# Kernel optimization log

Hardware: AMD Instinct MI355X
Metric: run time of the kernel (lower is better)

Reference implementation:

```python
import jax, jax.numpy as jnp
import numpy as np

NEG = -1e9  # stand-in for -inf in masked_fill; avoids NaN rows for never-gathered states


def _residual(x, w1, b1, w2, b2):
    # ResidualLayerOld: two relu linears with a residual connection (eval mode, no dropout)
    h = jax.nn.relu(x @ w1.T + b1)
    return x + jax.nn.relu(h @ w2.T + b2)


def setup_inputs() -> dict:
    key = jax.random.key(0)
    B, T, V, C, H, SPW = 16, 256, 32000, 1024, 512, 8
    ks = jax.random.split(key, 32)
    s = 0.05  # keep logits in a sane range
    inp = {
        'start_emb': jax.random.normal(ks[0], (C, H), jnp.float32) * s,
        'start_l1w': jax.random.normal(ks[1], (H, H), jnp.float32) * s,
        'start_l1b': jnp.zeros((H,), jnp.float32),
        'start_l2w': jax.random.normal(ks[2], (H, H), jnp.float32) * s,
        'start_l2b': jnp.zeros((H,), jnp.float32),
        'start_ow': jax.random.normal(ks[3], (1, H), jnp.float32) * s,
        'start_ob': jnp.zeros((1,), jnp.float32),
        'state_emb': jax.random.normal(ks[4], (C, H), jnp.float32) * s,
        'trans_l1w': jax.random.normal(ks[5], (H, H), jnp.float32) * s,
        'trans_l1b': jnp.zeros((H,), jnp.float32),
        'trans_l2w': jax.random.normal(ks[6], (H, H), jnp.float32) * s,
        'trans_l2b': jnp.zeros((H,), jnp.float32),
        'proj_w': jax.random.normal(ks[7], (C, H), jnp.float32) * s,
        'pret_emb': jax.random.normal(ks[8], (C, H), jnp.float32) * s,
        'term_l1w': jax.random.normal(ks[9], (H, H), jnp.float32) * s,
        'term_l1b': jnp.zeros((H,), jnp.float32),
        'term_l2w': jax.random.normal(ks[10], (H, H), jnp.float32) * s,
        'term_l2b': jnp.zeros((H,), jnp.float32),
        'term_ow': jax.random.normal(ks[11], (V, H), jnp.float32) * s,
        'term_ob': jnp.zeros((V,), jnp.float32),
        'text': jax.random.randint(ks[12], (B, T), 0, V, jnp.int32),
        'word2state': jax.random.randint(ks[13], (V, SPW), 0, C, jnp.int32),
    }
    return inp


def reference(start_emb, start_l1w, start_l1b, start_l2w, start_l2b, start_ow, start_ob,
              state_emb, trans_l1w, trans_l1b, trans_l2w, trans_l2b, proj_w,
              pret_emb, term_l1w, term_l1b, term_l2w, term_l2b, term_ow, term_ob,
              text, word2state):
    C, H = start_emb.shape
    V, SPW = word2state.shape

    # start: MLP(C,H)->(C,1) -> log_softmax over C
    start = jax.nn.log_softmax(
        (_residual(start_emb, start_l1w, start_l1b, start_l2w, start_l2b) @ start_ow.T + start_ob).squeeze(-1))

    # transition: [C,C] log_softmax over next state
    trans = jax.nn.log_softmax(
        _residual(state_emb, trans_l1w, trans_l1b, trans_l2w, trans_l2b) @ proj_w.T, axis=-1)

    # emission: [C,V] logits, masked to the sparse word->state assignment, log_softmax over V
    term_logits = _residual(pret_emb, term_l1w, term_l1b, term_l2w, term_l2b) @ term_ow.T + term_ob
    mask = jnp.zeros((C, V), bool).at[word2state.reshape(-1), jnp.repeat(jnp.arange(V), SPW)].set(True)
    emission = jax.nn.log_softmax(jnp.where(mask, term_logits, NEG), axis=-1)

    # clamp: gather per-timestep [SPW,SPW] transition blocks + emissions
    cs = word2state[text]                               # [B,T,SPW]
    pot = trans[cs[:, :-1, :, None], cs[:, 1:, None, :]]  # [B,T-1,SPW,SPW] (prev i, next j)
    init = start[cs[:, 0]]                              # [B,SPW]
    obs = emission[cs, text[:, :, None]]                # [B,T,SPW]
    pot = pot.at[:, 0].add((init + obs[:, 0])[:, :, None])
    pot = pot + obs[:, 1:][:, :, None, :]               # add obs_{t+1} along next-state j
    pot = jnp.swapaxes(pot, -1, -2)                     # [B,T-1,next,prev], as in clamp()

    # forward algorithm (fb kernel's alpha pass): alpha_{t+1}[n] = LSE_p pot[t,n,p] + alpha_t[p]
    def step(alpha, p):
        a = jax.nn.logsumexp(p + alpha[:, None, :], axis=-1)
        return a, None

    B = text.shape[0]
    alpha0 = jnp.zeros((B, SPW), pot.dtype)
    alphaT, _ = jax.lax.scan(step, alpha0, jnp.swapaxes(pot, 0, 1))
    evidence = jax.nn.logsumexp(alphaT, axis=-1).sum()  # full-length sequences
    return evidence
```

## Files before the change

### kernel.cpp

```cpp
#include <hip/hip_runtime.h>
#include <hip/hip_bf16.h>

#define C_DIM 1024
#define H_DIM 512
#define V_DIM 32000
#define B_DIM 16
#define T_DIM 256
#define SPW   8
#define NSLOT 32

typedef unsigned short u16;
typedef unsigned int   u32;
typedef __attribute__((ext_vector_type(8))) short bf16x8;
typedef __attribute__((ext_vector_type(4))) float f32x4;

__device__ __forceinline__ u16 f2b(float f) {
    union { float f; u32 i; } x; x.f = f;
    u32 i = x.i;
    i += 0x7fffu + ((i >> 16) & 1u);
    return (u16)(i >> 16);
}
__device__ __forceinline__ float b2f(u16 u) {
    union { u32 i; float f; } x; x.i = ((u32)u) << 16; return x.f;
}
__device__ __forceinline__ float dot8_bf16(uint4 u, const float4 tw0, const float4 tw1) {
    return tw0.x * b2f((u16)(u.x & 0xffff)) + tw0.y * b2f((u16)(u.x >> 16))
         + tw0.z * b2f((u16)(u.y & 0xffff)) + tw0.w * b2f((u16)(u.y >> 16))
         + tw1.x * b2f((u16)(u.z & 0xffff)) + tw1.y * b2f((u16)(u.z >> 16))
         + tw1.z * b2f((u16)(u.w & 0xffff)) + tw1.w * b2f((u16)(u.w >> 16));
}

struct CvtArgs {
    const float* src[10];
    u16*         dst[10];
    int          n[10];
    float*       zero;
    int          zn;
};

__global__ __launch_bounds__(256) void cvt_kern(CvtArgs a)
{
    int seg = blockIdx.y;
    if (seg == 10) {
        for (int i = blockIdx.x * 256 + threadIdx.x; i < a.zn; i += gridDim.x * 256)
            a.zero[i] = 0.0f;
        return;
    }
    const float4* s = (const float4*)a.src[seg];
    ushort4* d = (ushort4*)a.dst[seg];
    int n4 = a.n[seg] >> 2;
    for (int i = blockIdx.x * 256 + threadIdx.x; i < n4; i += gridDim.x * 256) {
        float4 v = s[i];
        ushort4 o;
        o.x = f2b(v.x); o.y = f2b(v.y); o.z = f2b(v.z); o.w = f2b(v.w);
        d[i] = o;
    }
}

struct MlpArgs {
    const u16*   A[3];
    const u16*   W[3];
    const float* bias[3];
    const float* resid[3];
    u16*         out[3];
};

__global__ __launch_bounds__(256) void mlp16_kern(MlpArgs args)
{
    const int N = H_DIM, K = H_DIM;
    int z = blockIdx.z;
    const u16* A = args.A[z];
    const u16* B = args.W[z];
    const float* bias = args.bias[z];
    const float* resid = args.resid[z];
    u16* out = args.out[z];

    __shared__ __align__(16) u16 As[2][64][40];
    __shared__ __align__(16) u16 Bs[2][64][40];
    int tid  = threadIdx.x;
    int m0 = blockIdx.x * 64, n0 = blockIdx.y * 64;
    int wave = tid >> 6, lane = tid & 63;
    int wr = wave >> 1, wc = wave & 1;
    int srow = tid >> 2, scol = (tid & 3) << 3;
    int quad = lane >> 4, l16 = lane & 15;
    f32x4 acc[2][2] = {};

    const u16* ap = A + (size_t)(m0 + srow) * K + scol;
    const u16* bp = B + (size_t)(n0 + srow) * K + scol;

    *(uint4*)&As[0][srow][scol] = *(const uint4*)ap;
    *(uint4*)&Bs[0][srow][scol] = *(const uint4*)bp;
    __syncthreads();
    int cur = 0;
#pragma unroll 1
    for (int k0 = 0; k0 + 32 < K; k0 += 32) {
        uint4 an = *(const uint4*)(ap + k0 + 32);
        uint4 bn = *(const uint4*)(bp + k0 + 32);
        bf16x8 af0 = *(const bf16x8*)&As[cur][wr * 32 + l16][quad * 8];
        bf16x8 af1 = *(const bf16x8*)&As[cur][wr * 32 + 16 + l16][quad * 8];
        bf16x8 bf0 = *(const bf16x8*)&Bs[cur][wc * 32 + l16][quad * 8];
        bf16x8 bf1 = *(const bf16x8*)&Bs[cur][wc * 32 + 16 + l16][quad * 8];
        acc[0][0] = __builtin_amdgcn_mfma_f32_16x16x32_bf16(af0, bf0, acc[0][0], 0, 0, 0);
        acc[0][1] = __builtin_amdgcn_mfma_f32_16x16x32_bf16(af0, bf1, acc[0][1], 0, 0, 0);
        acc[1][0] = __builtin_amdgcn_mfma_f32_16x16x32_bf16(af1, bf0, acc[1][0], 0, 0, 0);
        acc[1][1] = __builtin_amdgcn_mfma_f32_16x16x32_bf16(af1, bf1, acc[1][1], 0, 0, 0);
        *(uint4*)&As[cur ^ 1][srow][scol] = an;
        *(uint4*)&Bs[cur ^ 1][srow][scol] = bn;
        __syncthreads();
        cur ^= 1;
    }
    {
        bf16x8 af0 = *(const bf16x8*)&As[cur][wr * 32 + l16][quad * 8];
        bf16x8 af1 = *(const bf16x8*)&As[cur][wr * 32 + 16 + l16][quad * 8];
        bf16x8 bf0 = *(const bf16x8*)&Bs[cur][wc * 32 + l16][quad * 8];
        bf16x8 bf1 = *(const bf16x8*)&Bs[cur][wc * 32 + 16 + l16][quad * 8];
        acc[0][0] = __builtin_amdgcn_mfma_f32_16x16x32_bf16(af0, bf0, acc[0][0], 0, 0, 0);
        acc[0][1] = __builtin_amdgcn_mfma_f32_16x16x32_bf16(af0, bf1, acc[0][1], 0, 0, 0);
        acc[1][0] = __builtin_amdgcn_mfma_f32_16x16x32_bf16(af1, bf0, acc[1][0], 0, 0, 0);
        acc[1][1] = __builtin_amdgcn_mfma_f32_16x16x32_bf16(af1, bf1, acc[1][1], 0, 0, 0);
    }
#pragma unroll
    for (int sm = 0; sm < 2; sm++)
#pragma unroll
        for (int sn = 0; sn < 2; sn++) {
            int n = n0 + wc * 32 + sn * 16 + l16;
            float bv = bias[n];
#pragma unroll
            for (int reg = 0; reg < 4; reg++) {
                int m = m0 + wr * 32 + sm * 16 + quad * 4 + reg;
                float v = fmaxf(acc[sm][sn][reg] + bv, 0.0f);
                if (resid) v += resid[(size_t)m * N + n];
                out[(size_t)m * N + n] = f2b(v);
            }
        }
}

__global__ __launch_bounds__(256) void fused_mid_kern(
    const u16* __restrict__ Rtrans16, const u16* __restrict__ proj16,
    float* __restrict__ TL, float* __restrict__ rowsum,
    const u16* __restrict__ Rterm16, const float* __restrict__ tow,
    const float* __restrict__ tob, const int* __restrict__ w2s,
    float* __restrict__ Zpart, float* __restrict__ Lmat,
    const u16* __restrict__ Rstart16, const float* __restrict__ sow,
    const float* __restrict__ sob, float* __restrict__ startv,
    float* __restrict__ Ssum)
{
    __shared__ __align__(16) u16 As[2][64][40];
    __shared__ __align__(16) u16 Bs[2][64][40];
    int bx = blockIdx.x;
    int tid = threadIdx.x;
    int wid = tid >> 6, lane = tid & 63;

    if (bx < 256) {
        const int K = H_DIM;
        int m0 = (bx & 15) * 64, n0 = (bx >> 4) * 64;
        int wave = wid;
        int wr = wave >> 1, wc = wave & 1;
        int srow = tid >> 2, scol = (tid & 3) << 3;
        int quad = lane >> 4, l16 = lane & 15;
        f32x4 acc[2][2] = {};

        const u16* ap = Rtrans16 + (size_t)(m0 + srow) * K + scol;
        const u16* bp = proj16 + (size_t)(n0 + srow) * K + scol;

        *(uint4*)&As[0][srow][scol] = *(const uint4*)ap;
        *(uint4*)&Bs[0][srow][scol] = *(const uint4*)bp;
        __syncthreads();
        int cur = 0;
#pragma unroll 1
        for (int k0 = 0; k0 + 32 < K; k0 += 32) {
            uint4 an = *(const uint4*)(ap + k0 + 32);
            uint4 bn = *(const uint4*)(bp + k0 + 32);
            bf16x8 af0 = *(const bf16x8*)&As[cur][wr * 32 + l16][quad * 8];
            bf16x8 af1 = *(const bf16x8*)&As[cur][wr * 32 + 16 + l16][quad * 8];
            bf16x8 bf0 = *(const bf16x8*)&Bs[cur][wc * 32 + l16][quad * 8];
            bf16x8 bf1 = *(const bf16x8*)&Bs[cur][wc * 32 + 16 + l16][quad * 8];
            acc[0][0] = __builtin_amdgcn_mfma_f32_16x16x32_bf16(af0, bf0, acc[0][0], 0, 0, 0);
            acc[0][1] = __builtin_amdgcn_mfma_f32_16x16x32_bf16(af0, bf1, acc[0][1], 0, 0, 0);
            acc[1][0] = __builtin_amdgcn_mfma_f32_16x16x32_bf16(af1, bf0, acc[1][0], 0, 0, 0);
            acc[1][1] = __builtin_amdgcn_mfma_f32_16x16x32_bf16(af1, bf1, acc[1][1], 0, 0, 0);
            *(uint4*)&As[cur ^ 1][srow][scol] = an;
            *(uint4*)&Bs[cur ^ 1][srow][scol] = bn;
            __syncthreads();
            cur ^= 1;
        }
        {
            bf16x8 af0 = *(const bf16x8*)&As[cur][wr * 32 + l16][quad * 8];
            bf16x8 af1 = *(const bf16x8*)&As[cur][wr * 32 + 16 + l16][quad * 8];
            bf16x8 bf0 = *(const bf16x8*)&Bs[cur][wc * 32 + l16][quad * 8];
            bf16x8 bf1 = *(const bf16x8*)&Bs[cur][wc * 32 + 16 + l16][quad * 8];
            acc[0][0] = __builtin_amdgcn_mfma_f32_16x16x32_bf16(af0, bf0, acc[0][0], 0, 0, 0);
            acc[0][1] = __builtin_amdgcn_mfma_f32_16x16x32_bf16(af0, bf1, acc[0][1], 0, 0, 0);
            acc[1][0] = __builtin_amdgcn_mfma_f32_16x16x32_bf16(af1, bf0, acc[1][0], 0, 0, 0);
            acc[1][1] = __builtin_amdgcn_mfma_f32_16x16x32_bf16(af1, bf1, acc[1][1], 0, 0, 0);
        }
#pragma unroll
        for (int sm = 0; sm < 2; sm++)
#pragma unroll
            for (int reg = 0; reg < 4; reg++) {
                int m = m0 + wr * 32 + sm * 16 + quad * 4 + reg;
                float e = 0.0f;
#pragma unroll
                for (int sn = 0; sn < 2; sn++) {
                    int n = n0 + wc * 32 + sn * 16 + l16;
                    float v = acc[sm][sn][reg];
                    TL[(size_t)m * C_DIM + n] = v;
                    e += expf(v);
                }
                e += __shfl_xor(e, 1, 64);
                e += __shfl_xor(e, 2, 64);
                e += __shfl_xor(e, 4, 64);
                e += __shfl_xor(e, 8, 64);
                if (l16 == 0) atomicAdd(rowsum + m, e);
            }
        return;
    }

    if (bx < 256 + V_DIM / 4) {
        int vbid = bx - 256;
        int v = vbid * 4 + wid;
        float* slot = Zpart + (vbid & (NSLOT - 1)) * C_DIM;
        const float4* twp = (const float4*)(tow + (size_t)v * H_DIM);
        float4 tw0 = twp[lane * 2], tw1 = twp[lane * 2 + 1];
        float ob = tob[v];
        int cs[SPW];
#pragma unroll
        for (int s = 0; s < SPW; s++) cs[s] = w2s[v * SPW + s];
        uint4 rv[SPW];
#pragma unroll
        for (int s = 0; s < SPW; s++)
            rv[s] = ((const uint4*)(Rterm16 + (size_t)cs[s] * H_DIM))[lane];
        float d[SPW];
#pragma unroll
        for (int s = 0; s < SPW; s++) {
            d[s] = dot8_bf16(rv[s], tw0, tw1);
            d[s] += __shfl_xor(d[s], 1, 64);
            d[s] += __shfl_xor(d[s], 2, 64);
            d[s] += __shfl_xor(d[s], 4, 64);
        }
        float x = d[0];
        int myc = cs[0];
#pragma unroll
        for (int s = 1; s < SPW; s++) {
            if ((lane & 7) == s) { x = d[s]; myc = cs[s]; }
        }
        x += __shfl_xor(x, 8, 64);
        x += __shfl_xor(x, 16, 64);
        x += __shfl_xor(x, 32, 64);
        u32 dupmask = 0;
#pragma unroll
        for (int s = 1; s < SPW; s++) {
            bool dp = false;
#pragma unroll
            for (int s2 = 0; s2 < s; s2++) dp = dp || (cs[s2] == cs[s]);
            if (dp) dupmask |= (1u << s);
        }
        if (lane < 8) {
            Lmat[(size_t)v * SPW + lane] = x + ob;
            if (!((dupmask >> lane) & 1u))
                atomicAdd(slot + myc, expf(x + ob));
        }
        return;
    }

    int sbid = bx - (256 + V_DIM / 4);
    int c = sbid * 4 + wid;
    uint4 rv = ((const uint4*)(Rstart16 + (size_t)c * H_DIM))[lane];
    const float4* wp = (const float4*)(sow);
    float4 w0 = wp[lane * 2], w1 = wp[lane * 2 + 1];
    float d = dot8_bf16(rv, w0, w1);
    for (int off = 1; off < 64; off <<= 1) d += __shfl_xor(d, off, 64);
    if (lane == 0) {
        d += sob[0];
        startv[c] = d;
        atomicAdd(Ssum + (sbid & (NSLOT - 1)), expf(d));
    }
}

__global__ __launch_bounds__(256) void zred_kern(
    const float* __restrict__ Zpart, const float* __restrict__ rowsum,
    float* __restrict__ logZ, float* __restrict__ logrow)
{
    int c = blockIdx.x * 256 + threadIdx.x;
    float z = 0.0f;
#pragma unroll
    for (int k = 0; k < NSLOT; k++) z += Zpart[(size_t)k * C_DIM + c];
    logZ[c] = logf(z);
    logrow[c] = logf(rowsum[c]);
}

__device__ __forceinline__ float lsm_combine(float accv, float mv, int i, int j)
{
    float x[8];
#pragma unroll
    for (int k = 0; k < 8; k++) {
        float a = __shfl(accv, k * 8 + i, 64);
        float b = __shfl(mv,  j * 8 + k, 64);
        x[k] = a + b;
    }
    float mx = fmaxf(fmaxf(fmaxf(x[0], x[1]), fmaxf(x[2], x[3])),
                     fmaxf(fmaxf(x[4], x[5]), fmaxf(x[6], x[7])));
    float s = 0.0f;
#pragma unroll
    for (int k = 0; k < 8; k++) s += expf(x[k] - mx);
    return mx + logf(s);
}

__global__ __launch_bounds__(64) void scanA_kern(
    const float* __restrict__ TL, const float* __restrict__ logrow,
    const float* __restrict__ Lmat, const float* __restrict__ logZ,
    const float* __restrict__ startv, const float* __restrict__ Ssum,
    const int* __restrict__ text, const int* __restrict__ w2s,
    float* __restrict__ Mc)
{
    int lane = threadIdx.x;
    int g = blockIdx.x;
    int b = g >> 4, c = g & 15;
    int t0 = c * 16;
    int cnt = min(16, (T_DIM - 1) - t0);
    int i = lane & 7, j = lane >> 3;

    const int* txt = text + b * T_DIM;

    float logS = 0.0f;
    if (t0 == 0) {
        float ss = 0.0f;
#pragma unroll
        for (int k = 0; k < NSLOT; k++) ss += Ssum[k];
        logS = logf(ss);
    }

    auto potval = [&](int t) -> float {
        int vt  = txt[t];
        int vt1 = txt[t + 1];
        int ci = w2s[vt * SPW + i];
        int cj = w2s[vt1 * SPW + j];
        float p = TL[(size_t)ci * C_DIM + cj] - logrow[ci]
                + Lmat[(size_t)vt1 * SPW + j] - logZ[cj];
        if (t == 0)
            p += startv[ci] - logS + Lmat[(size_t)vt * SPW + i] - logZ[ci];
        return p;
    };

    float acc = potval(t0);
    if (cnt > 1) {
        float nv = potval(t0 + 1);
        for (int t = t0 + 1; t < t0 + cnt; t++) {
            float nv2 = (t + 1 < t0 + cnt) ? potval(t + 1) : 0.0f;
            acc = lsm_combine(acc, nv, i, j);
            nv = nv2;
        }
    }
    Mc[(size_t)g * 64 + lane] = acc;
}

__global__ __launch_bounds__(1024) void scanB_kern(const float* __restrict__ Mc,
                                                   float* __restrict__ out)
{
    int wave = threadIdx.x >> 6, lane = threadIdx.x & 63;
    int i = lane & 7, j = lane >> 3;
    const float* base = Mc + (size_t)wave * 16 * 64;
    float acc = base[lane];
    for (int c = 1; c < 16; c++)
        acc = lsm_combine(acc, base[(size_t)c * 64 + lane], i, j);
    float mx = acc;
    for (int o = 1; o < 64; o <<= 1) mx = fmaxf(mx, __shfl_xor(mx, o, 64));
    float e = expf(acc - mx);
    for (int o = 1; o < 64; o <<= 1) e += __shfl_xor(e, o, 64);
    __shared__ float part[16];
    if (lane == 0) part[wave] = mx + logf(e);
    __syncthreads();
    if (threadIdx.x == 0) {
        float s = 0.0f;
#pragma unroll
        for (int k = 0; k < 16; k++) s += part[k];
        out[0] = s;
    }
}

extern "C" void kernel_launch(void* const* d_in, const int* in_sizes, int n_in,
                              void* d_out, int out_size, void* d_ws, size_t ws_size,
                              hipStream_t stream)
{
    const float* start_emb = (const float*)d_in[0];
    const float* start_l1w = (const float*)d_in[1];
    const float* start_l1b = (const float*)d_in[2];
    const float* start_l2w = (const float*)d_in[3];
    const float* start_l2b = (const float*)d_in[4];
    const float* start_ow  = (const float*)d_in[5];
    const float* start_ob  = (const float*)d_in[6];
    const float* state_emb = (const float*)d_in[7];
    const float* trans_l1w = (const float*)d_in[8];
    const float* trans_l1b = (const float*)d_in[9];
    const float* trans_l2w = (const float*)d_in[10];
    const float* trans_l2b = (const float*)d_in[11];
    const float* proj_w    = (const float*)d_in[12];
    const float* pret_emb  = (const float*)d_in[13];
    const float* term_l1w  = (const float*)d_in[14];
    const float* term_l1b  = (const float*)d_in[15];
    const float* term_l2w  = (const float*)d_in[16];
    const float* term_l2b  = (const float*)d_in[17];
    const float* term_ow   = (const float*)d_in[18];
    const float* term_ob   = (const float*)d_in[19];
    const int*   text      = (const int*)d_in[20];
    const int*   w2s       = (const int*)d_in[21];

    char* w = (char*)d_ws;
    const u32 MB = 1u << 20;
    const size_t CH = (size_t)C_DIM * H_DIM;
    const size_t HH = (size_t)H_DIM * H_DIM;

    u16*   emb16  = (u16*)(w);
    u16*   w16    = (u16*)(w + 3u * MB);
    u16*   proj16 = (u16*)(w + 6u * MB);
    u16*   H16    = (u16*)(w + 7u * MB);
    u16*   R16    = (u16*)(w + 10u * MB);
    float* TL     = (float*)(w + 13u * MB);
    float* startv = (float*)(w + 17u * MB);
    float* logZ   = (float*)(w + 17u * MB + 4096);
    float* logrow = (float*)(w + 17u * MB + 8192);
    float* Mc     = (float*)(w + 17u * MB + 12288);
    float* Zpart  = (float*)(w + 18u * MB);
    float* Ssum   = Zpart + (size_t)NSLOT * C_DIM;
    float* rowsum = Ssum + NSLOT;
    float* Lmat   = (float*)(w + 19u * MB);

    u16* semb16 = emb16;
    u16* temb16 = emb16 + CH;
    u16* pemb16 = emb16 + 2 * CH;
    u16* sl1w16 = w16;
    u16* sl2w16 = w16 + HH;
    u16* tl1w16 = w16 + 2 * HH;
    u16* tl2w16 = w16 + 3 * HH;
    u16* ml1w16 = w16 + 4 * HH;
    u16* ml2w16 = w16 + 5 * HH;
    u16* Hs = H16, *Ht = H16 + CH, *Hp = H16 + 2 * CH;
    u16* Rstart16 = R16;
    u16* Rtrans16 = R16 + CH;
    u16* Rterm16  = R16 + 2 * CH;

    dim3 blk256(256);

    CvtArgs cv;
    cv.src[0] = start_emb; cv.dst[0] = semb16; cv.n[0] = (int)CH;
    cv.src[1] = state_emb; cv.dst[1] = temb16; cv.n[1] = (int)CH;
    cv.src[2] = pret_emb;  cv.dst[2] = pemb16; cv.n[2] = (int)CH;
    cv.src[3] = start_l1w; cv.dst[3] = sl1w16; cv.n[3] = (int)HH;
    cv.src[4] = start_l2w; cv.dst[4] = sl2w16; cv.n[4] = (int)HH;
    cv.src[5] = trans_l1w; cv.dst[5] = tl1w16; cv.n[5] = (int)HH;
    cv.src[6] = trans_l2w; cv.dst[6] = tl2w16; cv.n[6] = (int)HH;
    cv.src[7] = term_l1w;  cv.dst[7] = ml1w16; cv.n[7] = (int)HH;
    cv.src[8] = term_l2w;  cv.dst[8] = ml2w16; cv.n[8] = (int)HH;
    cv.src[9] = proj_w;    cv.dst[9] = proj16; cv.n[9] = (int)CH;
    cv.zero = Zpart; cv.zn = NSLOT * C_DIM + NSLOT + C_DIM;
    cvt_kern<<<dim3(128, 11), blk256, 0, stream>>>(cv);

    MlpArgs l1;
    l1.A[0] = semb16; l1.A[1] = temb16; l1.A[2] = pemb16;
    l1.W[0] = sl1w16; l1.W[1] = tl1w16; l1.W[2] = ml1w16;
    l1.bias[0] = start_l1b; l1.bias[1] = trans_l1b; l1.bias[2] = term_l1b;
    l1.resid[0] = nullptr; l1.resid[1] = nullptr; l1.resid[2] = nullptr;
    l1.out[0] = Hs; l1.out[1] = Ht; l1.out[2] = Hp;

    MlpArgs l2;
    l2.A[0] = Hs; l2.A[1] = Ht; l2.A[2] = Hp;
    l2.W[0] = sl2w16; l2.W[1] = tl2w16; l2.W[2] = ml2w16;
    l2.bias[0] = start_l2b; l2.bias[1] = trans_l2b; l2.bias[2] = term_l2b;
    l2.resid[0] = start_emb; l2.resid[1] = state_emb; l2.resid[2] = pret_emb;
    l2.out[0] = Rstart16; l2.out[1] = Rtrans16; l2.out[2] = Rterm16;

    mlp16_kern<<<dim3(16, 8, 3), blk256, 0, stream>>>(l1);
    mlp16_kern<<<dim3(16, 8, 3), blk256, 0, stream>>>(l2);

    fused_mid_kern<<<256 + V_DIM / 4 + C_DIM / 4, blk256, 0, stream>>>(
        Rtrans16, proj16, TL, rowsum,
        Rterm16, term_ow, term_ob, w2s, Zpart, Lmat,
        Rstart16, start_ow, start_ob, startv, Ssum);

    zred_kern<<<C_DIM / 256, blk256, 0, stream>>>(Zpart, rowsum, logZ, logrow);

    scanA_kern<<<B_DIM * 16, dim3(64), 0, stream>>>(TL, logrow, Lmat, logZ,
                                                    startv, Ssum, text, w2s, Mc);
    scanB_kern<<<1, 1024, 0, stream>>>(Mc, (float*)d_out);
}
```

Baseline: 226.0 us.

## Restructure pipeline: fold conversions into MLP, drop zred, finer scan segments

Moves the layer-2 weight and proj bf16 conversion into an extra z-slice of the first MLP launch, so it runs alongside the GEMM. The zred kernel is removed: scanA blocks each rebuild the log-normalisers in shared memory from a transposed Zpart layout. The vocabulary pass now handles two words per wave, and the fast __expf/__logf intrinsics replace expf/logf. Scan parallelism doubles to 32 segments per sequence with a per-batch tree reduction and an atomic add to the output. This trades redundant per-block normaliser work and lower-precision math for fewer launches and more parallelism.

```diff
diff --git a/kernel.cpp b/kernel.cpp
--- a/kernel.cpp
+++ b/kernel.cpp
@@ -8,6 +8,7 @@
 #define T_DIM 256
 #define SPW   8
 #define NSLOT 32
+#define NSEG  32
 
 typedef unsigned short u16;
 typedef unsigned int   u32;
@@ -31,19 +32,21 @@
 }
 
 struct CvtArgs {
-    const float* src[10];
-    u16*         dst[10];
-    int          n[10];
+    const float* src[6];
+    u16*         dst[6];
+    int          n[6];
     float*       zero;
     int          zn;
+    float*       out;
 };
 
 __global__ __launch_bounds__(256) void cvt_kern(CvtArgs a)
 {
     int seg = blockIdx.y;
-    if (seg == 10) {
+    if (seg == 6) {
         for (int i = blockIdx.x * 256 + threadIdx.x; i < a.zn; i += gridDim.x * 256)
             a.zero[i] = 0.0f;
+        if (blockIdx.x == 0 && threadIdx.x == 0) a.out[0] = 0.0f;
         return;
     }
     const float4* s = (const float4*)a.src[seg];
@@ -63,10 +66,30 @@
     const float* bias[3];
     const float* resid[3];
     u16*         out[3];
+    const float* csrc[4];
+    u16*         cdst[4];
+    int          cn[4];
 };
 
 __global__ __launch_bounds__(256) void mlp16_kern(MlpArgs args)
 {
+    if (blockIdx.z == 3) {
+        int idx = (blockIdx.y * gridDim.x + blockIdx.x) * 256 + threadIdx.x;
+        int stride = gridDim.x * gridDim.y * 256;
+#pragma unroll
+        for (int s = 0; s < 4; s++) {
+            const float4* sp = (const float4*)args.csrc[s];
+            ushort4* dp = (ushort4*)args.cdst[s];
+            int n4 = args.cn[s] >> 2;
+            for (int t = idx; t < n4; t += stride) {
+                float4 v = sp[t];
+                ushort4 o;
+                o.x = f2b(v.x); o.y = f2b(v.y); o.z = f2b(v.z); o.w = f2b(v.w);
+                dp[t] = o;
+            }
+        }
+        return;
+    }
     const int N = H_DIM, K = H_DIM;
     int z = blockIdx.z;
     const u16* A = args.A[z];
@@ -154,8 +177,7 @@
     if (bx < 256) {
         const int K = H_DIM;
         int m0 = (bx & 15) * 64, n0 = (bx >> 4) * 64;
-        int wave = wid;
-        int wr = wave >> 1, wc = wave & 1;
+        int wr = wid >> 1, wc = wid & 1;
         int srow = tid >> 2, scol = (tid & 3) << 3;
         int quad = lane >> 4, l16 = lane & 15;
         f32x4 acc[2][2] = {};
@@ -205,7 +227,7 @@
                     int n = n0 + wc * 32 + sn * 16 + l16;
                     float v = acc[sm][sn][reg];
                     TL[(size_t)m * C_DIM + n] = v;
-                    e += expf(v);
+                    e += __expf(v);
                 }
                 e += __shfl_xor(e, 1, 64);
                 e += __shfl_xor(e, 2, 64);
@@ -216,54 +238,57 @@
         return;
     }
 
-    if (bx < 256 + V_DIM / 4) {
-        int vbid = bx - 256;
-        int v = vbid * 4 + wid;
-        float* slot = Zpart + (vbid & (NSLOT - 1)) * C_DIM;
-        const float4* twp = (const float4*)(tow + (size_t)v * H_DIM);
-        float4 tw0 = twp[lane * 2], tw1 = twp[lane * 2 + 1];
-        float ob = tob[v];
-        int cs[SPW];
-#pragma unroll
-        for (int s = 0; s < SPW; s++) cs[s] = w2s[v * SPW + s];
-        uint4 rv[SPW];
-#pragma unroll
-        for (int s = 0; s < SPW; s++)
-            rv[s] = ((const uint4*)(Rterm16 + (size_t)cs[s] * H_DIM))[lane];
-        float d[SPW];
-#pragma unroll
-        for (int s = 0; s < SPW; s++) {
-            d[s] = dot8_bf16(rv[s], tw0, tw1);
-            d[s] += __shfl_xor(d[s], 1, 64);
-            d[s] += __shfl_xor(d[s], 2, 64);
-            d[s] += __shfl_xor(d[s], 4, 64);
-        }
-        float x = d[0];
-        int myc = cs[0];
-#pragma unroll
-        for (int s = 1; s < SPW; s++) {
-            if ((lane & 7) == s) { x = d[s]; myc = cs[s]; }
-        }
-        x += __shfl_xor(x, 8, 64);
-        x += __shfl_xor(x, 16, 64);
-        x += __shfl_xor(x, 32, 64);
-        u32 dupmask = 0;
-#pragma unroll
-        for (int s = 1; s < SPW; s++) {
-            bool dp = false;
-#pragma unroll
-            for (int s2 = 0; s2 < s; s2++) dp = dp || (cs[s2] == cs[s]);
-            if (dp) dupmask |= (1u << s);
-        }
-        if (lane < 8) {
-            Lmat[(size_t)v * SPW + lane] = x + ob;
-            if (!((dupmask >> lane) & 1u))
-                atomicAdd(slot + myc, expf(x + ob));
+    if (bx < 256 + V_DIM / 8) {
+        int qbid = bx - 256;
+        int slotid = qbid & (NSLOT - 1);
+#pragma unroll
+        for (int h = 0; h < 2; h++) {
+            int v = (qbid * 4 + wid) * 2 + h;
+            const float4* twp = (const float4*)(tow + (size_t)v * H_DIM);
+            float4 tw0 = twp[lane * 2], tw1 = twp[lane * 2 + 1];
+            float ob = tob[v];
+            int cs[SPW];
+#pragma unroll
+            for (int s = 0; s < SPW; s++) cs[s] = w2s[v * SPW + s];
+            uint4 rv[SPW];
+#pragma unroll
+            for (int s = 0; s < SPW; s++)
+                rv[s] = ((const uint4*)(Rterm16 + (size_t)cs[s] * H_DIM))[lane];
+            float d[SPW];
+#pragma unroll
+            for (int s = 0; s < SPW; s++) {
+                d[s] = dot8_bf16(rv[s], tw0, tw1);
+                d[s] += __shfl_xor(d[s], 1, 64);
+                d[s] += __shfl_xor(d[s], 2, 64);
+                d[s] += __shfl_xor(d[s], 4, 64);
+            }
+            float x = d[0];
+            int myc = cs[0];
+#pragma unroll
+            for (int s = 1; s < SPW; s++) {
+                if ((lane & 7) == s) { x = d[s]; myc = cs[s]; }
+            }
+            x += __shfl_xor(x, 8, 64);
+            x += __shfl_xor(x, 16, 64);
+            x += __shfl_xor(x, 32, 64);
+            u32 dupmask = 0;
+#pragma unroll
+            for (int s = 1; s < SPW; s++) {
+                bool dp = false;
+#pragma unroll
+                for (int s2 = 0; s2 < s; s2++) dp = dp || (cs[s2] == cs[s]);
+                if (dp) dupmask |= (1u << s);
+            }
+            if (lane < 8) {
+                Lmat[(size_t)v * SPW + lane] = x + ob;
+                if (!((dupmask >> lane) & 1u))
+                    atomicAdd(Zpart + (size_t)myc * NSLOT + slotid, __expf(x + ob));
+            }
         }
         return;
     }
 
-    int sbid = bx - (256 + V_DIM / 4);
+    int sbid = bx - (256 + V_DIM / 8);
     int c = sbid * 4 + wid;
     uint4 rv = ((const uint4*)(Rstart16 + (size_t)c * H_DIM))[lane];
     const float4* wp = (const float4*)(sow);
@@ -273,20 +298,8 @@
     if (lane == 0) {
         d += sob[0];
         startv[c] = d;
-        atomicAdd(Ssum + (sbid & (NSLOT - 1)), expf(d));
-    }
-}
-
-__global__ __launch_bounds__(256) void zred_kern(
-    const float* __restrict__ Zpart, const float* __restrict__ rowsum,
-    float* __restrict__ logZ, float* __restrict__ logrow)
-{
-    int c = blockIdx.x * 256 + threadIdx.x;
-    float z = 0.0f;
-#pragma unroll
-    for (int k = 0; k < NSLOT; k++) z += Zpart[(size_t)k * C_DIM + c];
-    logZ[c] = logf(z);
-    logrow[c] = logf(rowsum[c]);
+        atomicAdd(Ssum + (sbid & (NSLOT - 1)), __expf(d));
+    }
 }
 
 __device__ __forceinline__ float lsm_combine(float accv, float mv, int i, int j)
@@ -302,22 +315,37 @@
                      fmaxf(fmaxf(x[4], x[5]), fmaxf(x[6], x[7])));
     float s = 0.0f;
 #pragma unroll
-    for (int k = 0; k < 8; k++) s += expf(x[k] - mx);
-    return mx + logf(s);
+    for (int k = 0; k < 8; k++) s += __expf(x[k] - mx);
+    return mx + __logf(s);
 }
 
 __global__ __launch_bounds__(64) void scanA_kern(
-    const float* __restrict__ TL, const float* __restrict__ logrow,
-    const float* __restrict__ Lmat, const float* __restrict__ logZ,
+    const float* __restrict__ TL, const float* __restrict__ rowsum,
+    const float* __restrict__ Lmat, const float* __restrict__ Zpart,
     const float* __restrict__ startv, const float* __restrict__ Ssum,
     const int* __restrict__ text, const int* __restrict__ w2s,
     float* __restrict__ Mc)
 {
+    __shared__ float sLZ[C_DIM];
+    __shared__ float sLR[C_DIM];
     int lane = threadIdx.x;
+    for (int c = lane; c < C_DIM; c += 64) {
+        const float4* zp = (const float4*)(Zpart + (size_t)c * NSLOT);
+        float4 z0 = zp[0], z1 = zp[1], z2 = zp[2], z3 = zp[3];
+        float4 z4 = zp[4], z5 = zp[5], z6 = zp[6], z7 = zp[7];
+        float z = ((z0.x + z0.y + z0.z + z0.w) + (z1.x + z1.y + z1.z + z1.w))
+                + ((z2.x + z2.y + z2.z + z2.w) + (z3.x + z3.y + z3.z + z3.w))
+                + ((z4.x + z4.y + z4.z + z4.w) + (z5.x + z5.y + z5.z + z5.w))
+                + ((z6.x + z6.y + z6.z + z6.w) + (z7.x + z7.y + z7.z + z7.w));
+        sLZ[c] = __logf(z);
+        sLR[c] = __logf(rowsum[c]);
+    }
+    __syncthreads();
+
     int g = blockIdx.x;
-    int b = g >> 4, c = g & 15;
-    int t0 = c * 16;
-    int cnt = min(16, (T_DIM - 1) - t0);
+    int b = g >> 5, c = g & (NSEG - 1);
+    int t0 = c * ((T_DIM) / NSEG);
+    int cnt = min(T_DIM / NSEG, (T_DIM - 1) - t0);
     int i = lane & 7, j = lane >> 3;
 
     const int* txt = text + b * T_DIM;
@@ -327,7 +355,7 @@
         float ss = 0.0f;
 #pragma unroll
         for (int k = 0; k < NSLOT; k++) ss += Ssum[k];
-        logS = logf(ss);
+        logS = __logf(ss);
     }
 
     auto potval = [&](int t) -> float {
@@ -335,10 +363,10 @@
         int vt1 = txt[t + 1];
         int ci = w2s[vt * SPW + i];
         int cj = w2s[vt1 * SPW + j];
-        float p = TL[(size_t)ci * C_DIM + cj] - logrow[ci]
-                + Lmat[(size_t)vt1 * SPW + j] - logZ[cj];
+        float p = TL[(size_t)ci * C_DIM + cj] - sLR[ci]
+                + Lmat[(size_t)vt1 * SPW + j] - sLZ[cj];
         if (t == 0)
-            p += startv[ci] - logS + Lmat[(size_t)vt * SPW + i] - logZ[ci];
+            p += startv[ci] - logS + Lmat[(size_t)vt * SPW + i] - sLZ[ci];
         return p;
     };
 
@@ -354,27 +382,41 @@
     Mc[(size_t)g * 64 + lane] = acc;
 }
 
-__global__ __launch_bounds__(1024) void scanB_kern(const float* __restrict__ Mc,
-                                                   float* __restrict__ out)
-{
-    int wave = threadIdx.x >> 6, lane = threadIdx.x & 63;
+__global__ __launch_bounds__(512) void scanB_kern(const float* __restrict__ Mc,
+                                                  float* __restrict__ out)
+{
+    __shared__ float Lb[8][64];
+    int b = blockIdx.x;
+    int w = threadIdx.x >> 6, lane = threadIdx.x & 63;
     int i = lane & 7, j = lane >> 3;
-    const float* base = Mc + (size_t)wave * 16 * 64;
-    float acc = base[lane];
-    for (int c = 1; c < 16; c++)
-        acc = lsm_combine(acc, base[(size_t)c * 64 + lane], i, j);
-    float mx = acc;
-    for (int o = 1; o < 64; o <<= 1) mx = fmaxf(mx, __shfl_xor(mx, o, 64));
-    float e = expf(acc - mx);
-    for (int o = 1; o < 64; o <<= 1) e += __shfl_xor(e, o, 64);
-    __shared__ float part[16];
-    if (lane == 0) part[wave] = mx + logf(e);
-    __syncthreads();
-    if (threadIdx.x == 0) {
-        float s = 0.0f;
-#pragma unroll
-        for (int k = 0; k < 16; k++) s += part[k];
-        out[0] = s;
+    const float* base = Mc + (size_t)b * NSEG * 64;
+
+    float m0 = base[(size_t)(4 * w + 0) * 64 + lane];
+    float m1 = base[(size_t)(4 * w + 1) * 64 + lane];
+    float m2 = base[(size_t)(4 * w + 2) * 64 + lane];
+    float m3 = base[(size_t)(4 * w + 3) * 64 + lane];
+    float r01 = lsm_combine(m0, m1, i, j);
+    float r23 = lsm_combine(m2, m3, i, j);
+    float r = lsm_combine(r01, r23, i, j);
+    Lb[w][lane] = r;
+    __syncthreads();
+    float a, m;
+    if (w < 4) { a = Lb[2 * w][lane]; m = Lb[2 * w + 1][lane]; r = lsm_combine(a, m, i, j); }
+    __syncthreads();
+    if (w < 4) Lb[w][lane] = r;
+    __syncthreads();
+    if (w < 2) { a = Lb[2 * w][lane]; m = Lb[2 * w + 1][lane]; r = lsm_combine(a, m, i, j); }
+    __syncthreads();
+    if (w < 2) Lb[w][lane] = r;
+    __syncthreads();
+    if (w == 0) {
+        a = Lb[0][lane]; m = Lb[1][lane];
+        r = lsm_combine(a, m, i, j);
+        float mx = r;
+        for (int o = 1; o < 64; o <<= 1) mx = fmaxf(mx, __shfl_xor(mx, o, 64));
+        float e = __expf(r - mx);
+        for (int o = 1; o < 64; o <<= 1) e += __shfl_xor(e, o, 64);
+        if (lane == 0) atomicAdd(out, mx + __logf(e));
     }
 }
 
@@ -417,11 +459,9 @@
     u16*   R16    = (u16*)(w + 10u * MB);
     float* TL     = (float*)(w + 13u * MB);
     float* startv = (float*)(w + 17u * MB);
-    float* logZ   = (float*)(w + 17u * MB + 4096);
-    float* logrow = (float*)(w + 17u * MB + 8192);
-    float* Mc     = (float*)(w + 17u * MB + 12288);
+    float* Mc     = (float*)(w + 17u * MB + 4096);
     float* Zpart  = (float*)(w + 18u * MB);
-    float* Ssum   = Zpart + (size_t)NSLOT * C_DIM;
+    float* Ssum   = Zpart + (size_t)C_DIM * NSLOT;
     float* rowsum = Ssum + NSLOT;
     float* Lmat   = (float*)(w + 19u * MB);
 
@@ -446,14 +486,11 @@
     cv.src[1] = state_emb; cv.dst[1] = temb16; cv.n[1] = (int)CH;
     cv.src[2] = pret_emb;  cv.dst[2] = pemb16; cv.n[2] = (int)CH;
     cv.src[3] = start_l1w; cv.dst[3] = sl1w16; cv.n[3] = (int)HH;
-    cv.src[4] = start_l2w; cv.dst[4] = sl2w16; cv.n[4] = (int)HH;
-    cv.src[5] = trans_l1w; cv.dst[5] = tl1w16; cv.n[5] = (int)HH;
-    cv.src[6] = trans_l2w; cv.dst[6] = tl2w16; cv.n[6] = (int)HH;
-    cv.src[7] = term_l1w;  cv.dst[7] = ml1w16; cv.n[7] = (int)HH;
-    cv.src[8] = term_l2w;  cv.dst[8] = ml2w16; cv.n[8] = (int)HH;
-    cv.src[9] = proj_w;    cv.dst[9] = proj16; cv.n[9] = (int)CH;
-    cv.zero = Zpart; cv.zn = NSLOT * C_DIM + NSLOT + C_DIM;
-    cvt_kern<<<dim3(128, 11), blk256, 0, stream>>>(cv);
+    cv.src[4] = trans_l1w; cv.dst[4] = tl1w16; cv.n[4] = (int)HH;
+    cv.src[5] = term_l1w;  cv.dst[5] = ml1w16; cv.n[5] = (int)HH;
+    cv.zero = Zpart; cv.zn = C_DIM * NSLOT + NSLOT + C_DIM;
+    cv.out = (float*)d_out;
+    cvt_kern<<<dim3(64, 7), blk256, 0, stream>>>(cv);
 
     MlpArgs l1;
     l1.A[0] = semb16; l1.A[1] = temb16; l1.A[2] = pemb16;
@@ -461,6 +498,10 @@
     l1.bias[0] = start_l1b; l1.bias[1] = trans_l1b; l1.bias[2] = term_l1b;
     l1.resid[0] = nullptr; l1.resid[1] = nullptr; l1.resid[2] = nullptr;
     l1.out[0] = Hs; l1.out[1] = Ht; l1.out[2] = Hp;
+    l1.csrc[0] = start_l2w; l1.cdst[0] = sl2w16; l1.cn[0] = (int)HH;
+    l1.csrc[1] = trans_l2w; l1.cdst[1] = tl2w16; l1.cn[1] = (int)HH;
+    l1.csrc[2] = term_l2w;  l1.cdst[2] = ml2w16; l1.cn[2] = (int)HH;
+    l1.csrc[3] = proj_w;    l1.cdst[3] = proj16; l1.cn[3] = (int)CH;
 
     MlpArgs l2;
     l2.A[0] = Hs; l2.A[1] = Ht; l2.A[2] = Hp;
@@ -468,18 +509,20 @@
     l2.bias[0] = start_l2b; l2.bias[1] = trans_l2b; l2.bias[2] = term_l2b;
     l2.resid[0] = start_emb; l2.resid[1] = state_emb; l2.resid[2] = pret_emb;
     l2.out[0] = Rstart16; l2.out[1] = Rtrans16; l2.out[2] = Rterm16;
-
-    mlp16_kern<<<dim3(16, 8, 3), blk256, 0, stream>>>(l1);
+    l2.csrc[0] = nullptr; l2.cdst[0] = nullptr; l2.cn[0] = 0;
+    l2.csrc[1] = nullptr; l2.cdst[1] = nullptr; l2.cn[1] = 0;
+    l2.csrc[2] = nullptr; l2.cdst[2] = nullptr; l2.cn[2] = 0;
+    l2.csrc[3] = nullptr; l2.cdst[3] = nullptr; l2.cn[3] = 0;
+
+    mlp16_kern<<<dim3(16, 8, 4), blk256, 0, stream>>>(l1);
     mlp16_kern<<<dim3(16, 8, 3), blk256, 0, stream>>>(l2);
 
-    fused_mid_kern<<<256 + V_DIM / 4 + C_DIM / 4, blk256, 0, stream>>>(
+    fused_mid_kern<<<256 + V_DIM / 8 + C_DIM / 4, blk256, 0, stream>>>(
         Rtrans16, proj16, TL, rowsum,
         Rterm16, term_ow, term_ob, w2s, Zpart, Lmat,
         Rstart16, start_ow, start_ob, startv, Ssum);
 
-    zred_kern<<<C_DIM / 256, blk256, 0, stream>>>(Zpart, rowsum, logZ, logrow);
-
-    scanA_kern<<<B_DIM * 16, dim3(64), 0, stream>>>(TL, logrow, Lmat, logZ,
-                                                    startv, Ssum, text, w2s, Mc);
-    scanB_kern<<<1, 1024, 0, stream>>>(Mc, (float*)d_out);
-}
+    scanA_kern<<<B_DIM * NSEG, dim3(64), 0, stream>>>(TL, rowsum, Lmat, Zpart,
+                                                      startv, Ssum, text, w2s, Mc);
+    scanB_kern<<<B_DIM, dim3(512), 0, stream>>>(Mc, (float*)d_out);
+}
```

After: 212.3 us. 1.06x faster.
